# Kernel optimization log

Hardware: AMD Instinct MI355X
Metric: run time of the kernel (lower is better)

The kernel has to match this reference:

```python
import jax, jax.numpy as jnp
import numpy as np

E = 64       # hidden_dim
H = 8        # num_heads
D = E // H   # head_dim = 8
EPS = 1e-5


def _layernorm(x, g, b):
    mu = jnp.mean(x, axis=-1, keepdims=True)
    var = jnp.mean(jnp.square(x - mu), axis=-1, keepdims=True)
    return (x - mu) * jax.lax.rsqrt(var + EPS) * g + b


def setup_inputs() -> dict:
    key = jax.random.key(0)
    ks = jax.random.split(key, 16)
    B, Lq, Lk = 64, 512, 512
    s = 0.05  # param scale
    return {
        "q": jax.random.normal(ks[0], (B, Lq, E), jnp.float32),
        "k": jax.random.normal(ks[1], (B, Lk, E), jnp.float32),
        "prev_ga_output": jax.random.normal(ks[2], (B, Lq, E), jnp.float32),
        "Wq": jax.random.normal(ks[3], (E, E), jnp.float32) * s,
        "bq": jnp.zeros((E,), jnp.float32),
        "Wk": jax.random.normal(ks[4], (E, E), jnp.float32) * s,
        "bk": jnp.zeros((E,), jnp.float32),
        "Wv": jax.random.normal(ks[5], (E, E), jnp.float32) * s,
        "bv": jnp.zeros((E,), jnp.float32),
        "Wo": jax.random.normal(ks[6], (E, E), jnp.float32) * s,
        "bo": jnp.zeros((E,), jnp.float32),
        "ln1_g": jnp.ones((E,), jnp.float32),
        "ln1_b": jnp.zeros((E,), jnp.float32),
        "W1": jax.random.normal(ks[7], (E, E), jnp.float32) * s,
        "b1": jnp.zeros((E,), jnp.float32),
        "W2": jax.random.normal(ks[8], (E, E), jnp.float32) * s,
        "b2": jnp.zeros((E,), jnp.float32),
        "ln2_g": jnp.ones((E,), jnp.float32),
        "ln2_b": jnp.zeros((E,), jnp.float32),
    }


def reference(q, k, prev_ga_output, Wq, bq, Wk, bk, Wv, bv, Wo, bo,
              ln1_g, ln1_b, W1, b1, W2, b2, ln2_g, ln2_b):
    B, Lq, _ = q.shape
    Lk = k.shape[1]
    # projections (torch Linear convention: x @ W.T + b)
    qh = (q @ Wq.T + bq).reshape(B, Lq, H, D)
    kh = (k @ Wk.T + bk).reshape(B, Lk, H, D)
    vh = (k @ Wv.T + bv).reshape(B, Lk, H, D)
    scale = 1.0 / np.sqrt(D).astype(np.float32)
    scores = jnp.einsum('blhd,bmhd->bhlm', qh * scale, kh)  # [B,H,Lq,Lk]
    attn = jax.nn.softmax(scores, axis=-1)
    ctx = jnp.einsum('bhlm,bmhd->blhd', attn, vh).reshape(B, Lq, E)
    mha_out = ctx @ Wo.T + bo
    attn_wts = jnp.mean(attn, axis=1)  # average_attn_weights=True -> [B,Lq,Lk]
    x = _layernorm(mha_out + prev_ga_output, ln1_g, ln1_b)
    ff = jax.nn.relu(x @ W1.T + b1) @ W2.T + b2
    out = _layernorm(ff + x, ln2_g, ln2_b)
    return out, attn_wts
```

## Files before the change

kernel.cpp:

```cpp
#include <hip/hip_runtime.h>


using half4   = __attribute__((ext_vector_type(4))) _Float16;
using floatx4 = __attribute__((ext_vector_type(4))) float;

__global__ __launch_bounds__(256) void ga_proj(
    const float* __restrict__ q, const float* __restrict__ k,
    const float* __restrict__ Wq, const float* __restrict__ bq,
    const float* __restrict__ Wk, const float* __restrict__ bk,
    const float* __restrict__ Wv, const float* __restrict__ bv,
    _Float16* __restrict__ qws, _Float16* __restrict__ kfrag,
    _Float16* __restrict__ vfrag)
{
    const int type = blockIdx.y;
    const int row0 = blockIdx.x * 64;
    const float* __restrict__ src  = (type == 0) ? q : k;
    const float* __restrict__ W    = (type == 0) ? Wq : (type == 1) ? Wk : Wv;
    const float* __restrict__ bias = (type == 0) ? bq : (type == 1) ? bk : bv;

    __shared__ _Float16 xb16[64 * 72];
    __shared__ _Float16 wb16[64 * 72];

    const int t = threadIdx.x;
    #pragma unroll
    for (int j = 0; j < 4; ++j) {
        int f = t + 256 * j;
        int row = f >> 4, k0 = (f & 15) << 2;
        float4 v4 = *(const float4*)(src + (size_t)(row0 + row) * 64 + k0);
        half4 h4;
        h4[0] = (_Float16)v4.x; h4[1] = (_Float16)v4.y;
        h4[2] = (_Float16)v4.z; h4[3] = (_Float16)v4.w;
        *(half4*)&xb16[row * 72 + k0] = h4;
        float4 w4 = *(const float4*)(W + row * 64 + k0);
        half4 g4;
        g4[0] = (_Float16)w4.x; g4[1] = (_Float16)w4.y;
        g4[2] = (_Float16)w4.z; g4[3] = (_Float16)w4.w;
        *(half4*)&wb16[row * 72 + k0] = g4;
    }
    __syncthreads();

    const int lane = t & 63;
    const int w = t >> 6;
    const int quad = lane >> 4;
    const int l16 = lane & 15;
    const int m0 = w * 16;
    const int grow = row0 + m0;
    const int bb = grow >> 9;
    const int cc = (grow & 511) >> 4;
    const floatx4 zf4 = {0.f, 0.f, 0.f, 0.f};

    #pragma unroll
    for (int n = 0; n < 4; ++n) {
        floatx4 acc = zf4;
        #pragma unroll
        for (int kt = 0; kt < 4; ++kt) {
            half4 a4 = *(const half4*)&xb16[(m0 + l16) * 72 + kt * 16 + quad * 4];
            half4 b4 = *(const half4*)&wb16[(n * 16 + l16) * 72 + kt * 16 + quad * 4];
            acc = __builtin_amdgcn_mfma_f32_16x16x16f16(a4, b4, acc, 0, 0, 0);
        }
        const int e = n * 16 + l16;
        const float bv = bias[e];
        #pragma unroll
        for (int r = 0; r < 4; ++r) {
            float a = acc[r] + bv;
            if (type == 0) a *= 0.51012811866f;
            _Float16 hv = (_Float16)a;
            const int kk = quad * 4 + r;
            if (type == 0)
                qws[(size_t)(grow + kk) * 64 + e] = hv;
            else if (type == 1)
                kfrag[((size_t)(bb * 8 + (e >> 3)) * 32 + cc) * 128
                      + kk * 8 + (e & 7)] = hv;
            else
                vfrag[((size_t)(bb * 8 + (e >> 3)) * 32 + cc) * 128
                      + (e & 7) * 16 + kk] = hv;
        }
    }
}

__global__ __launch_bounds__(256, 4) void ga_attn(
    const _Float16* __restrict__ qws, const _Float16* __restrict__ kfrag,
    const _Float16* __restrict__ vfrag,
    const float* __restrict__ prev,
    const float* __restrict__ Wo, const float* __restrict__ bo,
    const float* __restrict__ ln1g, const float* __restrict__ ln1b,
    const float* __restrict__ W1, const float* __restrict__ b1,
    const float* __restrict__ W2, const float* __restrict__ b2,
    const float* __restrict__ ln2g, const float* __restrict__ ln2b,
    float* __restrict__ out, float* __restrict__ attn)
{
    __shared__ __align__(16) unsigned char smem[37632];
    _Float16* qb   = (_Float16*)smem;
    float*    inv8 = (float*)(smem + 2304);
    float*    ctxb = (float*)(smem + 2816);
    _Float16* xbf  = (_Float16*)(smem + 7168);
    _Float16* hbf  = (_Float16*)(smem + 9344);
    _Float16* wbf  = (_Float16*)(smem + 11520);

    const int t = threadIdx.x;
    const int lane = t & 63;
    const int w = t >> 6;
    const int quad = lane >> 4;
    const int l16 = lane & 15;
    const int b  = blockIdx.x & 63;
    const int l0 = (blockIdx.x >> 6) << 4;

    const _Float16* kfb = kfrag + (size_t)b * 32768;
    const _Float16* vfb = vfrag + (size_t)b * 32768;

    if (t < 128) {
        int row = t >> 3, off = (t & 7) << 3;
        *(float4*)&qb[row * 72 + off] =
            *(const float4*)(qws + ((size_t)b * 512 + l0 + row) * 64 + off);
    }
    #pragma unroll
    for (int i = 0; i < 3; ++i) {
        const float* Ws = (i == 0) ? Wo : (i == 1) ? W1 : W2;
        #pragma unroll
        for (int j = 0; j < 4; ++j) {
            int f = t + 256 * j;
            int e = f >> 4, k0 = (f & 15) << 2;
            float4 v4 = *(const float4*)(Ws + e * 64 + k0);
            half4 h4;
            h4[0] = (_Float16)v4.x; h4[1] = (_Float16)v4.y;
            h4[2] = (_Float16)v4.z; h4[3] = (_Float16)v4.w;
            *(half4*)&wbf[i * 4352 + e * 68 + k0] = h4;
        }
    }
    for (int i = t; i < 16 * 68; i += 256) ctxb[i] = 0.f;
    __syncthreads();

    const floatx4 zf4 = {0.f, 0.f, 0.f, 0.f};
    const _Float16 hz = (_Float16)0.f;

    #pragma unroll 1
    for (int hi = 0; hi < 2; ++hi) {
        const int h = hi * 4 + w;
        half4 bfrag = {hz, hz, hz, hz};
        if (quad < 2) bfrag = *(const half4*)&qb[l16 * 72 + h * 8 + quad * 4];
        const _Float16* kb = kfb + (size_t)h * 4096 + l16 * 8 + (quad & 1) * 4;
        float psum = 0.f;
        #pragma unroll 8
        for (int c = 0; c < 32; ++c) {
            half4 af = *(const half4*)(kb + c * 128);
            floatx4 sv = __builtin_amdgcn_mfma_f32_16x16x16f16(af, bfrag, zf4, 0, 0, 0);
            psum += (exp2f(sv[0]) + exp2f(sv[1])) + (exp2f(sv[2]) + exp2f(sv[3]));
        }
        psum += __shfl_xor(psum, 16);
        psum += __shfl_xor(psum, 32);
        if (lane < 16) inv8[h * 16 + l16] = 1.0f / psum;
    }
    __syncthreads();

    floatx4 attn_acc[8];
    #pragma unroll
    for (int i = 0; i < 8; ++i) attn_acc[i] = zf4;

    #pragma unroll 1
    for (int h = 0; h < 8; ++h) {
        half4 bfrag = {hz, hz, hz, hz};
        if (quad < 2) bfrag = *(const half4*)&qb[l16 * 72 + h * 8 + quad * 4];
        const float inv = inv8[h * 16 + l16];
        const _Float16* kb = kfb + ((size_t)h * 32 + w * 8) * 128 + l16 * 8 + (quad & 1) * 4;
        const _Float16* vb = vfb + ((size_t)h * 32 + w * 8) * 128 + (l16 & 7) * 16 + quad * 4;
        floatx4 cacc0 = zf4, cacc1 = zf4;
        #pragma unroll
        for (int c = 0; c < 8; ++c) {
            half4 af = *(const half4*)(kb + c * 128);
            floatx4 sv = __builtin_amdgcn_mfma_f32_16x16x16f16(af, bfrag, zf4, 0, 0, 0);
            float e0 = exp2f(sv[0]), e1 = exp2f(sv[1]);
            float e2 = exp2f(sv[2]), e3 = exp2f(sv[3]);
            floatx4 ev; ev[0] = e0 * inv; ev[1] = e1 * inv;
            ev[2] = e2 * inv; ev[3] = e3 * inv;
            attn_acc[c] += ev;
            half4 ph;
            ph[0] = (_Float16)e0; ph[1] = (_Float16)e1;
            ph[2] = (_Float16)e2; ph[3] = (_Float16)e3;
            half4 vf = *(const half4*)(vb + c * 128);
            if (c & 1) cacc1 = __builtin_amdgcn_mfma_f32_16x16x16f16(vf, ph, cacc1, 0, 0, 0);
            else       cacc0 = __builtin_amdgcn_mfma_f32_16x16x16f16(vf, ph, cacc0, 0, 0, 0);
        }
        floatx4 cs = (cacc0 + cacc1) * inv;
        if (quad < 2) {
            #pragma unroll
            for (int r = 0; r < 4; ++r)
                atomicAdd(&ctxb[l16 * 68 + h * 8 + quad * 4 + r], cs[r]);
        }
    }
    {
        float* ap = attn + ((size_t)b * 512 + l0 + l16) * 512 + w * 128 + quad * 4;
        #pragma unroll
        for (int c = 0; c < 8; ++c)
            *(floatx4*)(ap + c * 16) = attn_acc[c] * 0.125f;
    }
    __syncthreads();

    const int eo = lane;
    const float* pv = prev + ((size_t)b * 512 + l0) * 64;
    float xl[4];
    {
        float a0 = 0.f, a1 = 0.f, a2 = 0.f, a3 = 0.f;
        #pragma unroll
        for (int kq = 0; kq < 16; ++kq) {
            half4 w4 = *(const half4*)&wbf[eo * 68 + kq * 4];
            float w0 = (float)w4[0], w1 = (float)w4[1];
            float w2 = (float)w4[2], w3 = (float)w4[3];
            floatx4 x0 = *(const floatx4*)&ctxb[(w * 4 + 0) * 68 + kq * 4];
            floatx4 x1 = *(const floatx4*)&ctxb[(w * 4 + 1) * 68 + kq * 4];
            floatx4 x2 = *(const floatx4*)&ctxb[(w * 4 + 2) * 68 + kq * 4];
            floatx4 x3 = *(const floatx4*)&ctxb[(w * 4 + 3) * 68 + kq * 4];
            a0 = fmaf(x0[0], w0, a0); a0 = fmaf(x0[1], w1, a0);
            a0 = fmaf(x0[2], w2, a0); a0 = fmaf(x0[3], w3, a0);
            a1 = fmaf(x1[0], w0, a1); a1 = fmaf(x1[1], w1, a1);
            a1 = fmaf(x1[2], w2, a1); a1 = fmaf(x1[3], w3, a1);
            a2 = fmaf(x2[0], w0, a2); a2 = fmaf(x2[1], w1, a2);
            a2 = fmaf(x2[2], w2, a2); a2 = fmaf(x2[3], w3, a2);
            a3 = fmaf(x3[0], w0, a3); a3 = fmaf(x3[1], w1, a3);
            a3 = fmaf(x3[2], w2, a3); a3 = fmaf(x3[3], w3, a3);
        }
        const float bov = bo[eo], g1v = ln1g[eo], b1v = ln1b[eo];
        float av[4] = {a0, a1, a2, a3};
        #pragma unroll
        for (int p = 0; p < 4; ++p) {
            const int l = w * 4 + p;
            float a = av[p] + bov + pv[l * 64 + eo];
            float s1 = a, s2 = a * a;
            #pragma unroll
            for (int o = 1; o < 64; o <<= 1) { s1 += __shfl_xor(s1, o); s2 += __shfl_xor(s2, o); }
            float mu = s1 * (1.f / 64.f);
            float var = s2 * (1.f / 64.f) - mu * mu;
            float xn = (a - mu) * rsqrtf(var + 1e-5f) * g1v + b1v;
            xl[p] = xn;
            xbf[l * 68 + eo] = (_Float16)xn;
        }
    }
    {
        float a0 = 0.f, a1 = 0.f, a2 = 0.f, a3 = 0.f;
        #pragma unroll
        for (int kq = 0; kq < 16; ++kq) {
            half4 w4 = *(const half4*)&wbf[4352 + eo * 68 + kq * 4];
            float w0 = (float)w4[0], w1 = (float)w4[1];
            float w2 = (float)w4[2], w3 = (float)w4[3];
            half4 h0 = *(const half4*)&xbf[(w * 4 + 0) * 68 + kq * 4];
            half4 h1 = *(const half4*)&xbf[(w * 4 + 1) * 68 + kq * 4];
            half4 h2 = *(const half4*)&xbf[(w * 4 + 2) * 68 + kq * 4];
            half4 h3 = *(const half4*)&xbf[(w * 4 + 3) * 68 + kq * 4];
            a0 = fmaf((float)h0[0], w0, a0); a0 = fmaf((float)h0[1], w1, a0);
            a0 = fmaf((float)h0[2], w2, a0); a0 = fmaf((float)h0[3], w3, a0);
            a1 = fmaf((float)h1[0], w0, a1); a1 = fmaf((float)h1[1], w1, a1);
            a1 = fmaf((float)h1[2], w2, a1); a1 = fmaf((float)h1[3], w3, a1);
            a2 = fmaf((float)h2[0], w0, a2); a2 = fmaf((float)h2[1], w1, a2);
            a2 = fmaf((float)h2[2], w2, a2); a2 = fmaf((float)h2[3], w3, a2);
            a3 = fmaf((float)h3[0], w0, a3); a3 = fmaf((float)h3[1], w1, a3);
            a3 = fmaf((float)h3[2], w2, a3); a3 = fmaf((float)h3[3], w3, a3);
        }
        const float b1v = b1[eo];
        float av[4] = {a0, a1, a2, a3};
        #pragma unroll
        for (int p = 0; p < 4; ++p)
            hbf[(w * 4 + p) * 68 + eo] = (_Float16)fmaxf(av[p] + b1v, 0.f);
    }
    {
        float a0 = 0.f, a1 = 0.f, a2 = 0.f, a3 = 0.f;
        #pragma unroll
        for (int kq = 0; kq < 16; ++kq) {
            half4 w4 = *(const half4*)&wbf[8704 + eo * 68 + kq * 4];
            float w0 = (float)w4[0], w1 = (float)w4[1];
            float w2 = (float)w4[2], w3 = (float)w4[3];
            half4 h0 = *(const half4*)&hbf[(w * 4 + 0) * 68 + kq * 4];
            half4 h1 = *(const half4*)&hbf[(w * 4 + 1) * 68 + kq * 4];
            half4 h2 = *(const half4*)&hbf[(w * 4 + 2) * 68 + kq * 4];
            half4 h3 = *(const half4*)&hbf[(w * 4 + 3) * 68 + kq * 4];
            a0 = fmaf((float)h0[0], w0, a0); a0 = fmaf((float)h0[1], w1, a0);
            a0 = fmaf((float)h0[2], w2, a0); a0 = fmaf((float)h0[3], w3, a0);
            a1 = fmaf((float)h1[0], w0, a1); a1 = fmaf((float)h1[1], w1, a1);
            a1 = fmaf((float)h1[2], w2, a1); a1 = fmaf((float)h1[3], w3, a1);
            a2 = fmaf((float)h2[0], w0, a2); a2 = fmaf((float)h2[1], w1, a2);
            a2 = fmaf((float)h2[2], w2, a2); a2 = fmaf((float)h2[3], w3, a2);
            a3 = fmaf((float)h3[0], w0, a3); a3 = fmaf((float)h3[1], w1, a3);
            a3 = fmaf((float)h3[2], w2, a3); a3 = fmaf((float)h3[3], w3, a3);
        }
        const float b2v = b2[eo], g2v = ln2g[eo], be2v = ln2b[eo];
        float av[4] = {a0, a1, a2, a3};
        #pragma unroll
        for (int p = 0; p < 4; ++p) {
            const int l = w * 4 + p;
            float a = av[p] + b2v + xl[p];
            float s1 = a, s2 = a * a;
            #pragma unroll
            for (int o = 1; o < 64; o <<= 1) { s1 += __shfl_xor(s1, o); s2 += __shfl_xor(s2, o); }
            float mu = s1 * (1.f / 64.f);
            float var = s2 * (1.f / 64.f) - mu * mu;
            float xn = (a - mu) * rsqrtf(var + 1e-5f);
            out[((size_t)b * 512 + l0 + l) * 64 + eo] = xn * g2v + be2v;
        }
    }
}

extern "C" void kernel_launch(void* const* d_in, const int* in_sizes, int n_in,
                              void* d_out, int out_size, void* d_ws, size_t ws_size,
                              hipStream_t stream)
{
    (void)in_sizes; (void)n_in; (void)out_size; (void)ws_size;
    const float* q    = (const float*)d_in[0];
    const float* k    = (const float*)d_in[1];
    const float* prev = (const float*)d_in[2];
    const float* Wq   = (const float*)d_in[3];
    const float* bq   = (const float*)d_in[4];
    const float* Wk   = (const float*)d_in[5];
    const float* bk   = (const float*)d_in[6];
    const float* Wv   = (const float*)d_in[7];
    const float* bv   = (const float*)d_in[8];
    const float* Wo   = (const float*)d_in[9];
    const float* bo   = (const float*)d_in[10];
    const float* g1   = (const float*)d_in[11];
    const float* be1  = (const float*)d_in[12];
    const float* W1   = (const float*)d_in[13];
    const float* b1   = (const float*)d_in[14];
    const float* W2   = (const float*)d_in[15];
    const float* b2   = (const float*)d_in[16];
    const float* g2   = (const float*)d_in[17];
    const float* be2  = (const float*)d_in[18];

    float* out  = (float*)d_out;
    float* attn = out + (size_t)64 * 512 * 64;

    _Float16* qws   = (_Float16*)d_ws;
    _Float16* kfrag = qws   + (size_t)64 * 512 * 64;
    _Float16* vfrag = kfrag + (size_t)64 * 512 * 64;

    ga_proj<<<dim3(512, 3), 256, 0, stream>>>(q, k, Wq, bq, Wk, bk, Wv, bv,
                                              qws, kfrag, vfrag);
    ga_attn<<<dim3(2048), 256, 0, stream>>>(qws, kfrag, vfrag, prev, Wo, bo,
                                            g1, be1, W1, b1, W2, b2, g2, be2,
                                            out, attn);
}
```

Before: 218.8 us.

## Use MFMA for the output/FFN epilogue and drop shared-memory weight staging

The per-block epilogue (Wo projection, FFN W1/W2, and both layernorms) now runs on 16x16x16 fp16 MFMA instructions instead of scalar FMA loops. Weights are read straight from global memory (L2-resident) and converted per use, so they are no longer staged into shared memory. Shared memory per block drops from about 37 KB to 12 KB and the launch bound's occupancy hint rises from 4 to 6 blocks. Layernorm row reductions now use cross-wave partial sums in shared memory, which adds extra block barriers. The ctx input to Wo is also rounded to fp16, which slightly lowers precision.

```diff
diff --git a/kernel.cpp b/kernel.cpp
--- a/kernel.cpp
+++ b/kernel.cpp
@@ -78,7 +78,7 @@
     }
 }
 
-__global__ __launch_bounds__(256, 4) void ga_attn(
+__global__ __launch_bounds__(256, 6) void ga_attn(
     const _Float16* __restrict__ qws, const _Float16* __restrict__ kfrag,
     const _Float16* __restrict__ vfrag,
     const float* __restrict__ prev,
@@ -89,13 +89,14 @@
     const float* __restrict__ ln2g, const float* __restrict__ ln2b,
     float* __restrict__ out, float* __restrict__ attn)
 {
-    __shared__ __align__(16) unsigned char smem[37632];
+    __shared__ __align__(16) unsigned char smem[12288];
     _Float16* qb   = (_Float16*)smem;
     float*    inv8 = (float*)(smem + 2304);
     float*    ctxb = (float*)(smem + 2816);
     _Float16* xbf  = (_Float16*)(smem + 7168);
-    _Float16* hbf  = (_Float16*)(smem + 9344);
-    _Float16* wbf  = (_Float16*)(smem + 11520);
+    _Float16* hbf  = (_Float16*)(smem + 9472);
+    float*    lnp1 = (float*)(smem + 11776);
+    float*    lnp2 = (float*)(smem + 12032);
 
     const int t = threadIdx.x;
     const int lane = t & 63;
@@ -112,20 +113,6 @@
         int row = t >> 3, off = (t & 7) << 3;
         *(float4*)&qb[row * 72 + off] =
             *(const float4*)(qws + ((size_t)b * 512 + l0 + row) * 64 + off);
-    }
-    #pragma unroll
-    for (int i = 0; i < 3; ++i) {
-        const float* Ws = (i == 0) ? Wo : (i == 1) ? W1 : W2;
-        #pragma unroll
-        for (int j = 0; j < 4; ++j) {
-            int f = t + 256 * j;
-            int e = f >> 4, k0 = (f & 15) << 2;
-            float4 v4 = *(const float4*)(Ws + e * 64 + k0);
-            half4 h4;
-            h4[0] = (_Float16)v4.x; h4[1] = (_Float16)v4.y;
-            h4[2] = (_Float16)v4.z; h4[3] = (_Float16)v4.w;
-            *(half4*)&wbf[i * 4352 + e * 68 + k0] = h4;
-        }
     }
     for (int i = t; i < 16 * 68; i += 256) ctxb[i] = 0.f;
     __syncthreads();
@@ -195,104 +182,123 @@
     }
     __syncthreads();
 
-    const int eo = lane;
-    const float* pv = prev + ((size_t)b * 512 + l0) * 64;
-    float xl[4];
+    const int ecol = w * 16 + l16;
+    const size_t orow = (size_t)b * 512 + l0;
+    float y[4], xn[4];
+
     {
-        float a0 = 0.f, a1 = 0.f, a2 = 0.f, a3 = 0.f;
-        #pragma unroll
-        for (int kq = 0; kq < 16; ++kq) {
-            half4 w4 = *(const half4*)&wbf[eo * 68 + kq * 4];
-            float w0 = (float)w4[0], w1 = (float)w4[1];
-            float w2 = (float)w4[2], w3 = (float)w4[3];
-            floatx4 x0 = *(const floatx4*)&ctxb[(w * 4 + 0) * 68 + kq * 4];
-            floatx4 x1 = *(const floatx4*)&ctxb[(w * 4 + 1) * 68 + kq * 4];
-            floatx4 x2 = *(const floatx4*)&ctxb[(w * 4 + 2) * 68 + kq * 4];
-            floatx4 x3 = *(const floatx4*)&ctxb[(w * 4 + 3) * 68 + kq * 4];
-            a0 = fmaf(x0[0], w0, a0); a0 = fmaf(x0[1], w1, a0);
-            a0 = fmaf(x0[2], w2, a0); a0 = fmaf(x0[3], w3, a0);
-            a1 = fmaf(x1[0], w0, a1); a1 = fmaf(x1[1], w1, a1);
-            a1 = fmaf(x1[2], w2, a1); a1 = fmaf(x1[3], w3, a1);
-            a2 = fmaf(x2[0], w0, a2); a2 = fmaf(x2[1], w1, a2);
-            a2 = fmaf(x2[2], w2, a2); a2 = fmaf(x2[3], w3, a2);
-            a3 = fmaf(x3[0], w0, a3); a3 = fmaf(x3[1], w1, a3);
-            a3 = fmaf(x3[2], w2, a3); a3 = fmaf(x3[3], w3, a3);
-        }
-        const float bov = bo[eo], g1v = ln1g[eo], b1v = ln1b[eo];
-        float av[4] = {a0, a1, a2, a3};
-        #pragma unroll
-        for (int p = 0; p < 4; ++p) {
-            const int l = w * 4 + p;
-            float a = av[p] + bov + pv[l * 64 + eo];
-            float s1 = a, s2 = a * a;
-            #pragma unroll
-            for (int o = 1; o < 64; o <<= 1) { s1 += __shfl_xor(s1, o); s2 += __shfl_xor(s2, o); }
-            float mu = s1 * (1.f / 64.f);
-            float var = s2 * (1.f / 64.f) - mu * mu;
-            float xn = (a - mu) * rsqrtf(var + 1e-5f) * g1v + b1v;
-            xl[p] = xn;
-            xbf[l * 68 + eo] = (_Float16)xn;
-        }
-    }
+        floatx4 acc = zf4;
+        #pragma unroll
+        for (int kt = 0; kt < 4; ++kt) {
+            floatx4 cx = *(const floatx4*)&ctxb[l16 * 68 + kt * 16 + quad * 4];
+            half4 a4;
+            a4[0] = (_Float16)cx[0]; a4[1] = (_Float16)cx[1];
+            a4[2] = (_Float16)cx[2]; a4[3] = (_Float16)cx[3];
+            float4 wv = *(const float4*)(Wo + (size_t)ecol * 64 + kt * 16 + quad * 4);
+            half4 b4;
+            b4[0] = (_Float16)wv.x; b4[1] = (_Float16)wv.y;
+            b4[2] = (_Float16)wv.z; b4[3] = (_Float16)wv.w;
+            acc = __builtin_amdgcn_mfma_f32_16x16x16f16(a4, b4, acc, 0, 0, 0);
+        }
+        const float bov = bo[ecol], g1v = ln1g[ecol], b1v = ln1b[ecol];
+        float s1[4], s2[4];
+        #pragma unroll
+        for (int r = 0; r < 4; ++r) {
+            y[r] = acc[r] + bov + prev[(orow + quad * 4 + r) * 64 + ecol];
+            s1[r] = y[r]; s2[r] = y[r] * y[r];
+        }
+        #pragma unroll
+        for (int o = 1; o < 16; o <<= 1) {
+            #pragma unroll
+            for (int r = 0; r < 4; ++r) {
+                s1[r] += __shfl_xor(s1[r], o);
+                s2[r] += __shfl_xor(s2[r], o);
+            }
+        }
+        if (l16 == 0) {
+            #pragma unroll
+            for (int r = 0; r < 4; ++r) {
+                lnp1[(quad * 4 + r) * 4 + w] = s1[r];
+                lnp2[(quad * 4 + r) * 4 + w] = s2[r];
+            }
+        }
+        __syncthreads();
+        #pragma unroll
+        for (int r = 0; r < 4; ++r) {
+            floatx4 p1 = *(const floatx4*)&lnp1[(quad * 4 + r) * 4];
+            floatx4 p2 = *(const floatx4*)&lnp2[(quad * 4 + r) * 4];
+            float S1 = (p1[0] + p1[1]) + (p1[2] + p1[3]);
+            float S2 = (p2[0] + p2[1]) + (p2[2] + p2[3]);
+            float mu = S1 * (1.f / 64.f);
+            float var = S2 * (1.f / 64.f) - mu * mu;
+            xn[r] = (y[r] - mu) * rsqrtf(var + 1e-5f) * g1v + b1v;
+            xbf[(quad * 4 + r) * 72 + ecol] = (_Float16)xn[r];
+        }
+    }
+    __syncthreads();
+
     {
-        float a0 = 0.f, a1 = 0.f, a2 = 0.f, a3 = 0.f;
-        #pragma unroll
-        for (int kq = 0; kq < 16; ++kq) {
-            half4 w4 = *(const half4*)&wbf[4352 + eo * 68 + kq * 4];
-            float w0 = (float)w4[0], w1 = (float)w4[1];
-            float w2 = (float)w4[2], w3 = (float)w4[3];
-            half4 h0 = *(const half4*)&xbf[(w * 4 + 0) * 68 + kq * 4];
-            half4 h1 = *(const half4*)&xbf[(w * 4 + 1) * 68 + kq * 4];
-            half4 h2 = *(const half4*)&xbf[(w * 4 + 2) * 68 + kq * 4];
-            half4 h3 = *(const half4*)&xbf[(w * 4 + 3) * 68 + kq * 4];
-            a0 = fmaf((float)h0[0], w0, a0); a0 = fmaf((float)h0[1], w1, a0);
-            a0 = fmaf((float)h0[2], w2, a0); a0 = fmaf((float)h0[3], w3, a0);
-            a1 = fmaf((float)h1[0], w0, a1); a1 = fmaf((float)h1[1], w1, a1);
-            a1 = fmaf((float)h1[2], w2, a1); a1 = fmaf((float)h1[3], w3, a1);
-            a2 = fmaf((float)h2[0], w0, a2); a2 = fmaf((float)h2[1], w1, a2);
-            a2 = fmaf((float)h2[2], w2, a2); a2 = fmaf((float)h2[3], w3, a2);
-            a3 = fmaf((float)h3[0], w0, a3); a3 = fmaf((float)h3[1], w1, a3);
-            a3 = fmaf((float)h3[2], w2, a3); a3 = fmaf((float)h3[3], w3, a3);
-        }
-        const float b1v = b1[eo];
-        float av[4] = {a0, a1, a2, a3};
-        #pragma unroll
-        for (int p = 0; p < 4; ++p)
-            hbf[(w * 4 + p) * 68 + eo] = (_Float16)fmaxf(av[p] + b1v, 0.f);
-    }
+        floatx4 acc = zf4;
+        #pragma unroll
+        for (int kt = 0; kt < 4; ++kt) {
+            half4 a4 = *(const half4*)&xbf[l16 * 72 + kt * 16 + quad * 4];
+            float4 wv = *(const float4*)(W1 + (size_t)ecol * 64 + kt * 16 + quad * 4);
+            half4 b4;
+            b4[0] = (_Float16)wv.x; b4[1] = (_Float16)wv.y;
+            b4[2] = (_Float16)wv.z; b4[3] = (_Float16)wv.w;
+            acc = __builtin_amdgcn_mfma_f32_16x16x16f16(a4, b4, acc, 0, 0, 0);
+        }
+        const float b1v = b1[ecol];
+        #pragma unroll
+        for (int r = 0; r < 4; ++r)
+            hbf[(quad * 4 + r) * 72 + ecol] = (_Float16)fmaxf(acc[r] + b1v, 0.f);
+    }
+    __syncthreads();
+
     {
-        float a0 = 0.f, a1 = 0.f, a2 = 0.f, a3 = 0.f;
-        #pragma unroll
-        for (int kq = 0; kq < 16; ++kq) {
-            half4 w4 = *(const half4*)&wbf[8704 + eo * 68 + kq * 4];
-            float w0 = (float)w4[0], w1 = (float)w4[1];
-            float w2 = (float)w4[2], w3 = (float)w4[3];
-            half4 h0 = *(const half4*)&hbf[(w * 4 + 0) * 68 + kq * 4];
-            half4 h1 = *(const half4*)&hbf[(w * 4 + 1) * 68 + kq * 4];
-            half4 h2 = *(const half4*)&hbf[(w * 4 + 2) * 68 + kq * 4];
-            half4 h3 = *(const half4*)&hbf[(w * 4 + 3) * 68 + kq * 4];
-            a0 = fmaf((float)h0[0], w0, a0); a0 = fmaf((float)h0[1], w1, a0);
-            a0 = fmaf((float)h0[2], w2, a0); a0 = fmaf((float)h0[3], w3, a0);
-            a1 = fmaf((float)h1[0], w0, a1); a1 = fmaf((float)h1[1], w1, a1);
-            a1 = fmaf((float)h1[2], w2, a1); a1 = fmaf((float)h1[3], w3, a1);
-            a2 = fmaf((float)h2[0], w0, a2); a2 = fmaf((float)h2[1], w1, a2);
-            a2 = fmaf((float)h2[2], w2, a2); a2 = fmaf((float)h2[3], w3, a2);
-            a3 = fmaf((float)h3[0], w0, a3); a3 = fmaf((float)h3[1], w1, a3);
-            a3 = fmaf((float)h3[2], w2, a3); a3 = fmaf((float)h3[3], w3, a3);
-        }
-        const float b2v = b2[eo], g2v = ln2g[eo], be2v = ln2b[eo];
-        float av[4] = {a0, a1, a2, a3};
-        #pragma unroll
-        for (int p = 0; p < 4; ++p) {
-            const int l = w * 4 + p;
-            float a = av[p] + b2v + xl[p];
-            float s1 = a, s2 = a * a;
-            #pragma unroll
-            for (int o = 1; o < 64; o <<= 1) { s1 += __shfl_xor(s1, o); s2 += __shfl_xor(s2, o); }
-            float mu = s1 * (1.f / 64.f);
-            float var = s2 * (1.f / 64.f) - mu * mu;
-            float xn = (a - mu) * rsqrtf(var + 1e-5f);
-            out[((size_t)b * 512 + l0 + l) * 64 + eo] = xn * g2v + be2v;
+        floatx4 acc = zf4;
+        #pragma unroll
+        for (int kt = 0; kt < 4; ++kt) {
+            half4 a4 = *(const half4*)&hbf[l16 * 72 + kt * 16 + quad * 4];
+            float4 wv = *(const float4*)(W2 + (size_t)ecol * 64 + kt * 16 + quad * 4);
+            half4 b4;
+            b4[0] = (_Float16)wv.x; b4[1] = (_Float16)wv.y;
+            b4[2] = (_Float16)wv.z; b4[3] = (_Float16)wv.w;
+            acc = __builtin_amdgcn_mfma_f32_16x16x16f16(a4, b4, acc, 0, 0, 0);
+        }
+        const float b2v = b2[ecol], g2v = ln2g[ecol], be2v = ln2b[ecol];
+        float s1[4], s2[4];
+        #pragma unroll
+        for (int r = 0; r < 4; ++r) {
+            y[r] = acc[r] + b2v + xn[r];
+            s1[r] = y[r]; s2[r] = y[r] * y[r];
+        }
+        #pragma unroll
+        for (int o = 1; o < 16; o <<= 1) {
+            #pragma unroll
+            for (int r = 0; r < 4; ++r) {
+                s1[r] += __shfl_xor(s1[r], o);
+                s2[r] += __shfl_xor(s2[r], o);
+            }
+        }
+        if (l16 == 0) {
+            #pragma unroll
+            for (int r = 0; r < 4; ++r) {
+                lnp1[(quad * 4 + r) * 4 + w] = s1[r];
+                lnp2[(quad * 4 + r) * 4 + w] = s2[r];
+            }
+        }
+        __syncthreads();
+        #pragma unroll
+        for (int r = 0; r < 4; ++r) {
+            floatx4 p1 = *(const floatx4*)&lnp1[(quad * 4 + r) * 4];
+            floatx4 p2 = *(const floatx4*)&lnp2[(quad * 4 + r) * 4];
+            float S1 = (p1[0] + p1[1]) + (p1[2] + p1[3]);
+            float S2 = (p2[0] + p2[1]) + (p2[2] + p2[3]);
+            float mu = S1 * (1.f / 64.f);
+            float var = S2 * (1.f / 64.f) - mu * mu;
+            float o2 = (y[r] - mu) * rsqrtf(var + 1e-5f) * g2v + be2v;
+            out[(orow + quad * 4 + r) * 64 + ecol] = o2;
         }
     }
 }
```

Result: slower. 293.9 us (+34.4%).
